# Performance work log

Measured on AMD Instinct MI355X. Metric: run time of the kernel, lower is better.

Reference implementation:

```python
import jax, jax.numpy as jnp
import numpy as np
import math

SAMPLE_RATE = 16000
CUTOFF = 7500.0
Q = 0.707  # torchaudio default for lowpass_biquad

def _lowpass_biquad_coeffs(sample_rate, cutoff_freq, Q):
    w0 = 2.0 * math.pi * cutoff_freq / sample_rate
    alpha = math.sin(w0) / (2.0 * Q)
    cos_w0 = math.cos(w0)
    b0 = (1.0 - cos_w0) / 2.0
    b1 = 1.0 - cos_w0
    b2 = b0
    a0 = 1.0 + alpha
    a1 = -2.0 * cos_w0
    a2 = 1.0 - alpha
    # normalize by a0 (as torchaudio's biquad/lfilter does)
    return (b0 / a0, b1 / a0, b2 / a0, a1 / a0, a2 / a0)


def setup_inputs() -> dict:
    key = jax.random.key(0)
    x = jax.random.normal(key, (64, 320000), dtype=jnp.float32)
    return {"x": x}


def reference(x) -> jnp.ndarray:
    b0, b1, b2, a1, a2 = _lowpass_biquad_coeffs(SAMPLE_RATE, CUTOFF, Q)
    b0 = jnp.asarray(b0, x.dtype); b1 = jnp.asarray(b1, x.dtype)
    b2 = jnp.asarray(b2, x.dtype); a1 = jnp.asarray(a1, x.dtype)
    a2 = jnp.asarray(a2, x.dtype)

    B = x.shape[0]
    xT = jnp.swapaxes(x, 0, 1)  # [T, B] -> scan over time

    def step(carry, xn):
        x1, x2, y1, y2 = carry  # each [B]
        yn = b0 * xn + b1 * x1 + b2 * x2 - a1 * y1 - a2 * y2
        return (xn, x1, yn, y1), yn

    z = jnp.zeros((B,), x.dtype)
    _, yT = jax.lax.scan(step, (z, z, z, z), xT)
    return jnp.swapaxes(yT, 0, 1)  # [B, T]
```

## Files before the change

kernel.cpp:

```cpp
#include <hip/hip_runtime.h>
#include <cmath>

#ifndef M_PI
#define M_PI 3.14159265358979323846
#endif

constexpr int T_LEN  = 320000;
constexpr int B_ROWS = 64;
constexpr int CHUNK  = 32;
constexpr int VPT    = CHUNK / 4;
constexpr int NCHUNK = T_LEN / CHUNK;
constexpr int BLK_CHUNKS = 128;
constexpr int BLK_SPAN   = BLK_CHUNKS * CHUNK;
constexpr int HALO       = 3;
constexpr int HALO_VECS  = HALO * VPT;
constexpr int TILE_VECS  = HALO_VECS + BLK_CHUNKS * VPT;

__device__ __forceinline__ int swzv(int V) { return V ^ ((V >> 3) & 7); }

__device__ __forceinline__ float4 shfl_up4(float4 v, int d) {
  float4 r;
  r.x = __shfl_up(v.x, d); r.y = __shfl_up(v.y, d);
  r.z = __shfl_up(v.z, d); r.w = __shfl_up(v.w, d);
  return r;
}
__device__ __forceinline__ float4 bcast4(float4 v, int l) {
  float4 r;
  r.x = __shfl(v.x, l); r.y = __shfl(v.y, l);
  r.z = __shfl(v.z, l); r.w = __shfl(v.w, l);
  return r;
}

__global__ __launch_bounds__(256, 4) void biquad_shfl_kernel(
    const float* __restrict__ x, float* __restrict__ y,
    float b0, float b1, float b2, float a1, float a2,
    float q30, float p30, float q31, float p31) {
  const int b    = blockIdx.x;
  const int row  = blockIdx.y;
  const int t    = threadIdx.x;
  const int lane = t & 63;

  const int S       = b * BLK_SPAN;
  const int nchunks = min(BLK_CHUNKS, (T_LEN - S) / CHUNK);
  const int nvecs   = nchunks * VPT;
  const int ntot    = HALO_VECS + nvecs;

  const float* xr = x + (size_t)row * T_LEN;
  float*       yr = y + (size_t)row * T_LEN;

  __shared__ float4 tile[TILE_VECS];

  {
    const float4 z4 = make_float4(0.f, 0.f, 0.f, 0.f);
    float4 v0, v1, v2, v3, v4;
    if (b == 0) {
      const float4* g = reinterpret_cast<const float4*>(xr);
      v0 = (t >= HALO_VECS && t < ntot) ? g[t - HALO_VECS] : z4;
      v1 = (t + 256  < ntot) ? g[t + 256  - HALO_VECS] : z4;
      v2 = (t + 512  < ntot) ? g[t + 512  - HALO_VECS] : z4;
      v3 = (t + 768  < ntot) ? g[t + 768  - HALO_VECS] : z4;
      v4 = (t + 1024 < ntot) ? g[t + 1024 - HALO_VECS] : z4;
    } else {
      const float4* g = reinterpret_cast<const float4*>(xr + S - HALO * CHUNK);
      v0 = (t        < ntot) ? g[t]        : z4;
      v1 = (t + 256  < ntot) ? g[t + 256]  : z4;
      v2 = (t + 512  < ntot) ? g[t + 512]  : z4;
      v3 = (t + 768  < ntot) ? g[t + 768]  : z4;
      v4 = (t + 1024 < ntot) ? g[t + 1024] : z4;
    }
    if (t        < ntot) tile[swzv(t)]        = v0;
    if (t + 256  < ntot) tile[swzv(t + 256)]  = v1;
    if (t + 512  < ntot) tile[swzv(t + 512)]  = v2;
    if (t + 768  < ntot) tile[swzv(t + 768)]  = v3;
    if (t + 1024 < ntot) tile[swzv(t + 1024)] = v4;
  }
  __syncthreads();

  auto stepf = [&](float xn, float& X1, float& X2, float& Y1, float& Y2) -> float {
    float tt = fmaf(b2, X2, fmaf(b1, X1, b0 * xn));
    float u  = fmaf(-a2, Y2, tt);
    float yn = fmaf(-a1, Y1, u);
    X2 = X1; X1 = xn;
    Y2 = Y1; Y1 = yn;
    return yn;
  };

  float4 H = make_float4(0.f, 0.f, 0.f, 0.f);
  if (lane < 3) {
    const int hvb = HALO_VECS + ((t & ~63) - 3 + lane) * VPT;
    float hx1 = 0.f, hx2 = 0.f, hy1 = 0.f, hy2 = 0.f, hxl1 = 0.f, hxl2 = 0.f;
#pragma unroll
    for (int g2 = 0; g2 < 4; ++g2) {
      float4 ha = tile[swzv(hvb + 2 * g2)];
      float4 hb = tile[swzv(hvb + 2 * g2 + 1)];
      stepf(ha.x, hx1, hx2, hy1, hy2); stepf(ha.y, hx1, hx2, hy1, hy2);
      stepf(ha.z, hx1, hx2, hy1, hy2); stepf(ha.w, hx1, hx2, hy1, hy2);
      stepf(hb.x, hx1, hx2, hy1, hy2); stepf(hb.y, hx1, hx2, hy1, hy2);
      stepf(hb.z, hx1, hx2, hy1, hy2); stepf(hb.w, hx1, hx2, hy1, hy2);
      if (g2 == 3) { hxl1 = hb.w; hxl2 = hb.z; }
    }
    H = make_float4(hy1, hy2, hxl1, hxl2);
  }

  float4 m[VPT];
  const int vb = HALO_VECS + t * VPT;
#pragma unroll
  for (int k = 0; k < VPT; ++k) m[k] = tile[swzv(vb + k)];
  float xl1 = m[VPT - 1].w, xl2 = m[VPT - 1].z;
  {
    float x1 = 0.f, x2 = 0.f, y1 = 0.f, y2 = 0.f;
#pragma unroll
    for (int k = 0; k < VPT; ++k) {
      float4 v = m[k];
      m[k] = make_float4(stepf(v.x, x1, x2, y1, y2), stepf(v.y, x1, x2, y1, y2),
                         stepf(v.z, x1, x2, y1, y2), stepf(v.w, x1, x2, y1, y2));
    }
    float4 Sst = make_float4(y1, y2, xl1, xl2);
    float4 up1 = shfl_up4(Sst, 1);
    float4 up2 = shfl_up4(Sst, 2);
    float4 up3 = shfl_up4(Sst, 3);
    float4 H0 = bcast4(H, 0), H1 = bcast4(H, 1), H2 = bcast4(H, 2);
    float4 sm1 = (lane == 0) ? H2 : up1;
    float4 sm2 = (lane == 0) ? H1 : ((lane == 1) ? H2 : up2);
    float4 sm3 = (lane == 0) ? H0 : ((lane == 1) ? H1 : ((lane == 2) ? H2 : up3));

    float cA0 = fmaf(b1, sm3.z, fmaf(b2, sm3.w, fmaf(-a1, sm3.x, -a2 * sm3.y)));
    float cA1 = fmaf(-a1, cA0, fmaf(b2, sm3.z, -a2 * sm3.x));
    float yA1 = fmaf(q31, cA0, fmaf(p31, cA1, sm2.x));
    float yA2 = fmaf(q30, cA0, fmaf(p30, cA1, sm2.y));
    float cB0 = fmaf(b1, sm2.z, fmaf(b2, sm2.w, fmaf(-a1, yA1, -a2 * yA2)));
    float cB1 = fmaf(-a1, cB0, fmaf(b2, sm2.z, -a2 * yA1));
    float yB1 = fmaf(q31, cB0, fmaf(p31, cB1, sm1.x));
    float yB2 = fmaf(q30, cB0, fmaf(p30, cB1, sm1.y));
    float c0 = fmaf(b1, sm1.z, fmaf(b2, sm1.w, fmaf(-a1, yB1, -a2 * yB2)));
    float c1 = fmaf(-a1, c0, fmaf(b2, sm1.z, -a2 * yB1));
    float cm2, cm1;
    {
      m[0].x += c0; m[0].y += c1;
      float c2 = fmaf(-a1, c1, -a2 * c0); m[0].z += c2;
      float c3 = fmaf(-a1, c2, -a2 * c1); m[0].w += c3;
      cm2 = c2; cm1 = c3;
    }
#pragma unroll
    for (int k = 1; k < VPT; ++k) {
      float ca = fmaf(-a1, cm1, -a2 * cm2); m[k].x += ca;
      float cb = fmaf(-a1, ca, -a2 * cm1);  m[k].y += cb;
      float cc = fmaf(-a1, cb, -a2 * ca);   m[k].z += cc;
      float cd = fmaf(-a1, cc, -a2 * cb);   m[k].w += cd;
      cm2 = cc; cm1 = cd;
    }
  }
  if (t < nchunks) {
#pragma unroll
    for (int k = 0; k < VPT; ++k) tile[swzv(vb + k)] = m[k];
  }
  __syncthreads();

  {
    float4* dst = reinterpret_cast<float4*>(yr + S);
#pragma unroll
    for (int j = 0; j < 4; ++j) {
      int i = t + 256 * j;
      if (i < nvecs) dst[i] = tile[swzv(HALO_VECS + i)];
    }
  }
}

extern "C" void kernel_launch(void* const* d_in, const int* in_sizes, int n_in,
                              void* d_out, int out_size, void* d_ws, size_t ws_size,
                              hipStream_t stream) {
  const float* x = (const float*)d_in[0];
  float*       y = (float*)d_out;

  const double sample_rate = 16000.0, cutoff = 7500.0, Q = 0.707;
  double w0    = 2.0 * M_PI * cutoff / sample_rate;
  double alpha = sin(w0) / (2.0 * Q);
  double cw    = cos(w0);
  double a0    = 1.0 + alpha;
  double b0d = ((1.0 - cw) * 0.5) / a0;
  double b1d = (1.0 - cw) / a0;
  double a1d = (-2.0 * cw) / a0;
  double a2d = (1.0 - alpha) / a0;

  double qm2 = 1.0, pm2 = 0.0, qm1 = 0.0, pm1 = 1.0;
  double q30 = 0, p30 = 0, q31 = 0, p31 = 0;
  for (int n = 2; n < CHUNK; ++n) {
    double qn = -a1d * qm1 - a2d * qm2;
    double pn = -a1d * pm1 - a2d * pm2;
    qm2 = qm1; pm2 = pm1; qm1 = qn; pm1 = pn;
    if (n == 30) { q30 = qn; p30 = pn; }
    if (n == 31) { q31 = qn; p31 = pn; }
  }

  dim3 block(256);
  dim3 grid((NCHUNK + BLK_CHUNKS - 1) / BLK_CHUNKS, B_ROWS);
  hipLaunchKernelGGL(biquad_shfl_kernel, grid, block, 0, stream,
                     x, y, (float)b0d, (float)b1d, (float)b0d, (float)a1d, (float)a2d,
                     (float)q30, (float)p30, (float)q31, (float)p31);
}
```

Measured before the change: 34.47 us.

## Give each wave its own tile with halo and drop block-wide barriers

Each 64-lane wave now owns a private LDS region holding its 64 chunks plus a 3-chunk halo, loads it and writes it back itself, so both __syncthreads calls go away. Blocks shrink from 256 to 128 threads, giving more, smaller blocks. The cost is redundant halo loads for every wave instead of every block, and a little more global traffic. Correctness now depends on wave-level lockstep for LDS visibility without explicit barriers.

```diff
diff --git a/kernel.cpp b/kernel.cpp
--- a/kernel.cpp
+++ b/kernel.cpp
@@ -5,16 +5,17 @@
 #define M_PI 3.14159265358979323846
 #endif
 
-constexpr int T_LEN  = 320000;
-constexpr int B_ROWS = 64;
-constexpr int CHUNK  = 32;
-constexpr int VPT    = CHUNK / 4;
-constexpr int NCHUNK = T_LEN / CHUNK;
-constexpr int BLK_CHUNKS = 128;
-constexpr int BLK_SPAN   = BLK_CHUNKS * CHUNK;
-constexpr int HALO       = 3;
-constexpr int HALO_VECS  = HALO * VPT;
-constexpr int TILE_VECS  = HALO_VECS + BLK_CHUNKS * VPT;
+constexpr int T_LEN    = 320000;
+constexpr int ROW_VECS = T_LEN / 4;
+constexpr int B_ROWS   = 64;
+constexpr int CHUNK    = 32;
+constexpr int VPT      = CHUNK / 4;
+constexpr int NCHUNK   = T_LEN / CHUNK;
+constexpr int WCH      = 64;
+constexpr int WAVES_PB = 2;
+constexpr int HALO     = 3;
+constexpr int WAVE_VECS = (HALO + WCH) * VPT;
+constexpr int BLK_CH   = WAVES_PB * WCH;
 
 __device__ __forceinline__ int swzv(int V) { return V ^ ((V >> 3) & 7); }
 
@@ -31,50 +32,40 @@
   return r;
 }
 
-__global__ __launch_bounds__(256, 4) void biquad_shfl_kernel(
+__global__ __launch_bounds__(128, 4) void biquad_wave_kernel(
     const float* __restrict__ x, float* __restrict__ y,
     float b0, float b1, float b2, float a1, float a2,
     float q30, float p30, float q31, float p31) {
   const int b    = blockIdx.x;
   const int row  = blockIdx.y;
   const int t    = threadIdx.x;
+  const int w    = t >> 6;
   const int lane = t & 63;
 
-  const int S       = b * BLK_SPAN;
-  const int nchunks = min(BLK_CHUNKS, (T_LEN - S) / CHUNK);
-  const int nvecs   = nchunks * VPT;
-  const int ntot    = HALO_VECS + nvecs;
+  const int CW = (b * WAVES_PB + w) * WCH;
+  const int wb = w * WAVE_VECS;
 
-  const float* xr = x + (size_t)row * T_LEN;
-  float*       yr = y + (size_t)row * T_LEN;
+  const float4* xr4 = reinterpret_cast<const float4*>(x + (size_t)row * T_LEN);
+  float4*       yr4 = reinterpret_cast<float4*>(y + (size_t)row * T_LEN);
 
-  __shared__ float4 tile[TILE_VECS];
+  __shared__ float4 tile[WAVES_PB * WAVE_VECS];
 
   {
     const float4 z4 = make_float4(0.f, 0.f, 0.f, 0.f);
-    float4 v0, v1, v2, v3, v4;
-    if (b == 0) {
-      const float4* g = reinterpret_cast<const float4*>(xr);
-      v0 = (t >= HALO_VECS && t < ntot) ? g[t - HALO_VECS] : z4;
-      v1 = (t + 256  < ntot) ? g[t + 256  - HALO_VECS] : z4;
-      v2 = (t + 512  < ntot) ? g[t + 512  - HALO_VECS] : z4;
-      v3 = (t + 768  < ntot) ? g[t + 768  - HALO_VECS] : z4;
-      v4 = (t + 1024 < ntot) ? g[t + 1024 - HALO_VECS] : z4;
-    } else {
-      const float4* g = reinterpret_cast<const float4*>(xr + S - HALO * CHUNK);
-      v0 = (t        < ntot) ? g[t]        : z4;
-      v1 = (t + 256  < ntot) ? g[t + 256]  : z4;
-      v2 = (t + 512  < ntot) ? g[t + 512]  : z4;
-      v3 = (t + 768  < ntot) ? g[t + 768]  : z4;
-      v4 = (t + 1024 < ntot) ? g[t + 1024] : z4;
+    const int gbase = CW * VPT - HALO * VPT;
+    float4 val[9];
+#pragma unroll
+    for (int j = 0; j < 9; ++j) {
+      int v = j * 64 + lane;
+      int g = gbase + v;
+      val[j] = (v < WAVE_VECS && g >= 0 && g < ROW_VECS) ? xr4[g] : z4;
     }
-    if (t        < ntot) tile[swzv(t)]        = v0;
-    if (t + 256  < ntot) tile[swzv(t + 256)]  = v1;
-    if (t + 512  < ntot) tile[swzv(t + 512)]  = v2;
-    if (t + 768  < ntot) tile[swzv(t + 768)]  = v3;
-    if (t + 1024 < ntot) tile[swzv(t + 1024)] = v4;
+#pragma unroll
+    for (int j = 0; j < 9; ++j) {
+      int v = j * 64 + lane;
+      if (v < WAVE_VECS) tile[wb + swzv(v)] = val[j];
+    }
   }
-  __syncthreads();
 
   auto stepf = [&](float xn, float& X1, float& X2, float& Y1, float& Y2) -> float {
     float tt = fmaf(b2, X2, fmaf(b1, X1, b0 * xn));
@@ -86,28 +77,25 @@
   };
 
   float4 H = make_float4(0.f, 0.f, 0.f, 0.f);
-  if (lane < 3) {
-    const int hvb = HALO_VECS + ((t & ~63) - 3 + lane) * VPT;
+  if (lane < HALO) {
+    const int hvb = lane * VPT;
     float hx1 = 0.f, hx2 = 0.f, hy1 = 0.f, hy2 = 0.f, hxl1 = 0.f, hxl2 = 0.f;
 #pragma unroll
-    for (int g2 = 0; g2 < 4; ++g2) {
-      float4 ha = tile[swzv(hvb + 2 * g2)];
-      float4 hb = tile[swzv(hvb + 2 * g2 + 1)];
-      stepf(ha.x, hx1, hx2, hy1, hy2); stepf(ha.y, hx1, hx2, hy1, hy2);
-      stepf(ha.z, hx1, hx2, hy1, hy2); stepf(ha.w, hx1, hx2, hy1, hy2);
-      stepf(hb.x, hx1, hx2, hy1, hy2); stepf(hb.y, hx1, hx2, hy1, hy2);
-      stepf(hb.z, hx1, hx2, hy1, hy2); stepf(hb.w, hx1, hx2, hy1, hy2);
-      if (g2 == 3) { hxl1 = hb.w; hxl2 = hb.z; }
+    for (int k = 0; k < VPT; ++k) {
+      float4 hv = tile[wb + swzv(hvb + k)];
+      stepf(hv.x, hx1, hx2, hy1, hy2); stepf(hv.y, hx1, hx2, hy1, hy2);
+      stepf(hv.z, hx1, hx2, hy1, hy2); stepf(hv.w, hx1, hx2, hy1, hy2);
+      if (k == VPT - 1) { hxl1 = hv.w; hxl2 = hv.z; }
     }
     H = make_float4(hy1, hy2, hxl1, hxl2);
   }
 
   float4 m[VPT];
-  const int vb = HALO_VECS + t * VPT;
+  const int mvb = (HALO + lane) * VPT;
 #pragma unroll
-  for (int k = 0; k < VPT; ++k) m[k] = tile[swzv(vb + k)];
-  float xl1 = m[VPT - 1].w, xl2 = m[VPT - 1].z;
+  for (int k = 0; k < VPT; ++k) m[k] = tile[wb + swzv(mvb + k)];
   {
+    float xl1 = m[VPT - 1].w, xl2 = m[VPT - 1].z;
     float x1 = 0.f, x2 = 0.f, y1 = 0.f, y2 = 0.f;
 #pragma unroll
     for (int k = 0; k < VPT; ++k) {
@@ -115,6 +103,7 @@
       m[k] = make_float4(stepf(v.x, x1, x2, y1, y2), stepf(v.y, x1, x2, y1, y2),
                          stepf(v.z, x1, x2, y1, y2), stepf(v.w, x1, x2, y1, y2));
     }
+
     float4 Sst = make_float4(y1, y2, xl1, xl2);
     float4 up1 = shfl_up4(Sst, 1);
     float4 up2 = shfl_up4(Sst, 2);
@@ -150,18 +139,19 @@
       cm2 = cc; cm1 = cd;
     }
   }
-  if (t < nchunks) {
+
 #pragma unroll
-    for (int k = 0; k < VPT; ++k) tile[swzv(vb + k)] = m[k];
-  }
-  __syncthreads();
+  for (int k = 0; k < VPT; ++k) tile[wb + swzv(mvb + k)] = m[k];
 
   {
-    float4* dst = reinterpret_cast<float4*>(yr + S);
+    float4 o[8];
 #pragma unroll
-    for (int j = 0; j < 4; ++j) {
-      int i = t + 256 * j;
-      if (i < nvecs) dst[i] = tile[swzv(HALO_VECS + i)];
+    for (int j = 0; j < 8; ++j)
+      o[j] = tile[wb + swzv(HALO * VPT + j * 64 + lane)];
+#pragma unroll
+    for (int j = 0; j < 8; ++j) {
+      int ov = CW * VPT + j * 64 + lane;
+      if (ov < ROW_VECS) yr4[ov] = o[j];
     }
   }
 }
@@ -192,9 +182,9 @@
     if (n == 31) { q31 = qn; p31 = pn; }
   }
 
-  dim3 block(256);
-  dim3 grid((NCHUNK + BLK_CHUNKS - 1) / BLK_CHUNKS, B_ROWS);
-  hipLaunchKernelGGL(biquad_shfl_kernel, grid, block, 0, stream,
+  dim3 block(128);
+  dim3 grid((NCHUNK + BLK_CH - 1) / BLK_CH, B_ROWS);
+  hipLaunchKernelGGL(biquad_wave_kernel, grid, block, 0, stream,
                      x, y, (float)b0d, (float)b1d, (float)b0d, (float)a1d, (float)a2d,
                      (float)q30, (float)p30, (float)q31, (float)p31);
 }
```

Measured after the change: 36.17 us. +4.9%, slower.
